# Performance work log

Hardware: AMD Instinct MI355X
Metric: run time of the kernel (lower is better)

Reference implementation:

```python
import jax, jax.numpy as jnp
import numpy as np

S, N, C_M, C_Z, C, H = 256, 384, 64, 128, 32, 8


def _layer_norm(x, w, b, eps=1e-5):
    mu = x.mean(axis=-1, keepdims=True)
    var = x.var(axis=-1, keepdims=True)
    return (x - mu) / jnp.sqrt(var + eps) * w + b


def setup_inputs() -> dict:
    key = jax.random.key(0)
    ks = jax.random.split(key, 8)
    m = jax.random.normal(ks[0], (S, N, C_M), dtype=jnp.float32)
    z = jax.random.normal(ks[1], (N, N, C_Z), dtype=jnp.float32)
    single_mask = jax.random.bernoulli(ks[2], 0.9, (N,))
    scale = 0.02
    return {
        "m": m,
        "z": z,
        "single_mask": single_mask,
        "ln_m_w": jnp.ones((C_M,), jnp.float32),
        "ln_m_b": jnp.zeros((C_M,), jnp.float32),
        "ln_z_w": jnp.ones((C_Z,), jnp.float32),
        "ln_z_b": jnp.zeros((C_Z,), jnp.float32),
        "w_v": jax.random.normal(ks[3], (C_M, H * C), jnp.float32) * scale,
        "w_b": jax.random.normal(ks[4], (C_Z, H), jnp.float32) * scale,
        "w_g": jax.random.normal(ks[5], (C_M, H * C), jnp.float32) * scale,
        "w_out": jax.random.normal(ks[6], (H * C, C_M), jnp.float32) * scale,
    }


def reference(m, z, single_mask, ln_m_w, ln_m_b, ln_z_w, ln_z_b, w_v, w_b, w_g, w_out):
    # m: [s, i, c_m], z: [i, j, c_z], single_mask: [j] bool
    m_ln = _layer_norm(m, ln_m_w, ln_m_b)
    v = (m_ln @ w_v).reshape(S, N, H, C)          # [s, j, h, c]
    b = _layer_norm(z, ln_z_w, ln_z_b) @ w_b      # [i, j, h]
    g = jax.nn.sigmoid(m_ln @ w_g)                # [s, i, h*c]
    # mask broadcast over j axis: [..., None, :, None]
    b = b + jnp.where(single_mask[None, :, None], 0.0, -1e9)
    w = jax.nn.softmax(b, axis=-2)                # softmax over j
    o = jnp.einsum('ijh,sjhc->sihc', w, v)        # [s, i, h, c]
    o = g * o.reshape(S, N, H * C)
    return o @ w_out                               # [s, i, c_m]
```

## Files before the change

kernel.cpp:

```cpp
#include <hip/hip_runtime.h>
#include <math.h>


#define SS 256
#define NN 384
#define CM 64
#define CZ 128
#define HH 8
#define HC 256
#define NV 25165824

typedef __attribute__((ext_vector_type(8))) short short8v;
typedef __attribute__((ext_vector_type(8))) unsigned short ushort8v;
typedef __attribute__((ext_vector_type(4))) unsigned short ushort4v;
typedef __attribute__((ext_vector_type(4))) float f32x4;

static __device__ __forceinline__ float bf2f(unsigned short u) {
    union { unsigned int i; float f; } x; x.i = ((unsigned int)u) << 16; return x.f;
}
static __device__ __forceinline__ unsigned short f2bf(float f) {
    union { float f; unsigned int i; } x; x.f = f;
    unsigned int r = x.i + 0x7FFFu + ((x.i >> 16) & 1u);
    return (unsigned short)(r >> 16);
}
static __device__ __forceinline__ void gload_lds16(const void* g, void* l) {
    __builtin_amdgcn_global_load_lds((const __attribute__((address_space(1))) void*)g,
                                     (__attribute__((address_space(3))) void*)l, 16, 0, 0);
}

__global__ __launch_bounds__(384) void k0_mask(const unsigned int* __restrict__ mu,
                                               float* __restrict__ mterm)
{
    __shared__ int byteLayout;
    if (threadIdx.x == 0) byteLayout = 0;
    __syncthreads();
    if (threadIdx.x < 96) {
        unsigned int u = mu[threadIdx.x];
        if (u != 0u && u != 1u && u != 0x3F800000u) atomicOr(&byteLayout, 1);
    }
    __syncthreads();
    const int j = threadIdx.x;
    int val;
    if (byteLayout) val = ((const unsigned char*)mu)[j];
    else            val = (mu[j] != 0u);
    mterm[j] = val ? 0.0f : -1e9f;
}

__global__ __launch_bounds__(256) void k1a_stageB(
    const float* __restrict__ w_v, const float* __restrict__ w_g,
    unsigned short* __restrict__ BTg)
{
    const int col = blockIdx.x * 4 + (threadIdx.x >> 6);
    const int k   = threadIdx.x & 63;
    float w = (col < 256) ? w_v[k * 256 + col] : w_g[k * 256 + (col - 256)];
    BTg[col * 64 + (k ^ ((col & 7) << 3))] = f2bf(w);
}

__global__ __launch_bounds__(128) void k2a_stageW(
    const float* __restrict__ lnw, const float* __restrict__ lnb, const float* __restrict__ w_b,
    unsigned short* __restrict__ w2bf, float* __restrict__ consts)
{
    __shared__ float pA[128][8], pB[128][8];
    const int c = threadIdx.x;
    float lw = lnw[c], lb = lnb[c];
    float4 wb0 = *(const float4*)&w_b[c * 8];
    float4 wb1 = *(const float4*)&w_b[c * 8 + 4];
    float wv[8] = {wb0.x, wb0.y, wb0.z, wb0.w, wb1.x, wb1.y, wb1.z, wb1.w};
    #pragma unroll
    for (int h = 0; h < 8; h++) {
        w2bf[h * CZ + c]       = f2bf(lw * wv[h]);
        w2bf[(8 + h) * CZ + c] = 0;
        pA[c][h] = lw * wv[h];
        pB[c][h] = lb * wv[h];
    }
    __syncthreads();
    if (c < 8) {
        float A = 0.f, B = 0.f;
        for (int q = 0; q < 128; q++) { A += pA[q][c]; B += pB[q][c]; }
        consts[c] = A; consts[16 + c] = B;
        consts[8 + c] = 0.f; consts[24 + c] = 0.f;
    }
}

__global__ __launch_bounds__(256) void k1n_ln(
    const float* __restrict__ m, const float* __restrict__ lnw, const float* __restrict__ lnb,
    unsigned short* __restrict__ mln)
{
    const int tid = threadIdx.x, wid = tid >> 6, lane = tid & 63;
    const int rowBase = blockIdx.x * 64 + wid * 16;
    const float lw = lnw[lane], lb = lnb[lane];
    #pragma unroll 4
    for (int rr = 0; rr < 16; rr++) {
        int row = rowBase + rr;
        float x = m[(size_t)row * CM + lane];
        float s1 = x, s2 = x * x;
        #pragma unroll
        for (int off = 32; off; off >>= 1) {
            s1 += __shfl_xor(s1, off);
            s2 += __shfl_xor(s2, off);
        }
        float mu  = s1 * (1.0f / CM);
        float var = s2 * (1.0f / CM) - mu * mu;
        float y = (x - mu) * rsqrtf(var + 1e-5f) * lw + lb;
        mln[(size_t)row * CM + (lane ^ ((row & 7) << 3))] = f2bf(y);
    }
}

__global__ __launch_bounds__(256) void k1b_vg(
    const unsigned short* __restrict__ BTg, const unsigned short* __restrict__ mln,
    unsigned short* __restrict__ vT, unsigned short* __restrict__ gout)
{
    __shared__ unsigned short Wl[32768];
    __shared__ unsigned short Al[4096];
    const int tid = threadIdx.x, wid = tid >> 6, lane = tid & 63;
    const int rl = lane & 15, kc = lane >> 4;
    const int rowBase = blockIdx.x * 64;
    const int s = rowBase / NN, j0 = rowBase - s * NN;

    #pragma unroll
    for (int it = 0; it < 16; it++) {
        int eoff = (wid * 16 + it) * 512;
        gload_lds16(BTg + eoff + lane * 8, (void*)((char*)Wl + eoff * 2));
    }
    #pragma unroll
    for (int it = 0; it < 2; it++) {
        int eoff = (wid * 2 + it) * 512;
        gload_lds16(mln + (size_t)rowBase * CM + eoff + lane * 8, (void*)((char*)Al + eoff * 2));
    }
    __syncthreads();

    short8v al[2][4];
    #pragma unroll
    for (int ks = 0; ks < 2; ks++)
        #pragma unroll
        for (int q = 0; q < 4; q++) {
            int row = q * 16 + rl;
            al[ks][q] = *(const short8v*)&Al[(row * 64 + ks * 32 + kc * 8) ^ ((row & 7) << 3)];
        }

    {
        f32x4 acc[4][4] = {};
        #pragma unroll
        for (int ks = 0; ks < 2; ks++) {
            short8v wf[4];
            #pragma unroll
            for (int q = 0; q < 4; q++) {
                int col = wid * 64 + q * 16 + rl;
                wf[q] = *(const short8v*)&Wl[(col * 64 + ks * 32 + kc * 8) ^ ((col & 7) << 3)];
            }
            #pragma unroll
            for (int mi = 0; mi < 4; mi++)
                #pragma unroll
                for (int nf = 0; nf < 4; nf++)
                    acc[mi][nf] = __builtin_amdgcn_mfma_f32_16x16x32_bf16(al[ks][mi], wf[nf], acc[mi][nf], 0, 0, 0);
        }
        #pragma unroll
        for (int mi = 0; mi < 4; mi++) {
            const int jb = j0 + mi * 16 + kc * 4;
            #pragma unroll
            for (int nf = 0; nf < 4; nf++) {
                int hc = wid * 64 + nf * 16 + rl;
                size_t vrow = (size_t)((hc >> 5) * 8192 + s * 32 + (hc & 31));
                ushort4v o4;
                #pragma unroll
                for (int r = 0; r < 4; r++) o4[r] = f2bf(acc[mi][nf][r]);
                *(ushort4v*)&vT[vrow * NN + jb] = o4;
            }
        }
    }

    {
        f32x4 acc[4][4] = {};
        #pragma unroll
        for (int ks = 0; ks < 2; ks++) {
            short8v wf[4];
            #pragma unroll
            for (int q = 0; q < 4; q++) {
                int col = 256 + wid * 64 + q * 16 + rl;
                wf[q] = *(const short8v*)&Wl[(col * 64 + ks * 32 + kc * 8) ^ ((col & 7) << 3)];
            }
            #pragma unroll
            for (int mi = 0; mi < 4; mi++)
                #pragma unroll
                for (int nf = 0; nf < 4; nf++)
                    acc[mi][nf] = __builtin_amdgcn_mfma_f32_16x16x32_bf16(wf[mi], al[ks][nf], acc[mi][nf], 0, 0, 0);
        }
        #pragma unroll
        for (int mi = 0; mi < 4; mi++) {
            const int hcb = wid * 64 + mi * 16 + kc * 4;
            #pragma unroll
            for (int nf = 0; nf < 4; nf++) {
                int row = rowBase + nf * 16 + rl;
                ushort4v o4;
                #pragma unroll
                for (int r = 0; r < 4; r++)
                    o4[r] = f2bf(1.0f / (1.0f + expf(-acc[mi][nf][r])));
                *(ushort4v*)&gout[(size_t)row * HC + hcb] = o4;
            }
        }
    }
}

__global__ __launch_bounds__(256) void k2_mfma(
    const float* __restrict__ z, const unsigned short* __restrict__ w2bf,
    const float* __restrict__ consts, const float* __restrict__ mterm,
    unsigned short* __restrict__ wbl)
{
    __shared__ float st[4][16][2];
    const int tid = threadIdx.x, wid = tid >> 6, lane = tid & 63;
    const int rl = lane & 15, kc = lane >> 4;
    const int rowBase = blockIdx.x * 64 + wid * 16;
    const int i = rowBase / NN, j0 = rowBase - i * NN;
    const float* zr = z + (size_t)(rowBase + rl) * CZ + kc * 8;

    float s1 = 0.f, s2 = 0.f;
    short8v af[4];
    #pragma unroll
    for (int ks = 0; ks < 4; ks++) {
        float4 z0 = *(const float4*)(zr + ks * 32);
        float4 z1 = *(const float4*)(zr + ks * 32 + 4);
        float zz[8] = {z0.x, z0.y, z0.z, z0.w, z1.x, z1.y, z1.z, z1.w};
        short8v a;
        #pragma unroll
        for (int q = 0; q < 8; q++) {
            s1 += zz[q];
            s2 += zz[q] * zz[q];
            a[q] = (short)f2bf(zz[q]);
        }
        af[ks] = a;
    }
    s1 += __shfl_xor(s1, 16); s2 += __shfl_xor(s2, 16);
    s1 += __shfl_xor(s1, 32); s2 += __shfl_xor(s2, 32);
    if (kc == 0) { st[wid][rl][0] = s1; st[wid][rl][1] = s2; }

    f32x4 acc = {};
    #pragma unroll
    for (int ks = 0; ks < 4; ks++) {
        short8v b = *(const short8v*)&w2bf[rl * CZ + ks * 32 + kc * 8];
        acc = __builtin_amdgcn_mfma_f32_16x16x32_bf16(af[ks], b, acc, 0, 0, 0);
    }
    __syncthreads();

    const float Ah = consts[rl], Bh = consts[16 + rl];
    unsigned short pv[4];
    #pragma unroll
    for (int reg = 0; reg < 4; reg++) {
        int r = 4 * kc + reg;
        float S1 = st[wid][r][0], S2 = st[wid][r][1];
        float mu   = S1 * (1.0f / CZ);
        float var  = S2 * (1.0f / CZ) - mu * mu;
        float rstd = rsqrtf(var + 1e-5f);
        float b = rstd * acc[reg] - rstd * mu * Ah + Bh + mterm[j0 + r];
        pv[reg] = f2bf(b);
    }
    if (rl < 8) {
        ushort4v o4 = {pv[0], pv[1], pv[2], pv[3]};
        *(ushort4v*)&wbl[((size_t)rl * NN + i) * NN + j0 + 4 * kc] = o4;
    }
}

__global__ __launch_bounds__(256) void k3_softmax(unsigned short* __restrict__ wbl)
{
    const int tid = threadIdx.x, wave = tid >> 6, lane = tid & 63;
    const int row = blockIdx.x * 4 + wave;
    unsigned short* p = wbl + (size_t)row * NN;
    float x[6];
    float mx = -1e30f;
    #pragma unroll
    for (int e = 0; e < 6; e++) { x[e] = bf2f(p[lane + e * 64]); mx = fmaxf(mx, x[e]); }
    #pragma unroll
    for (int off = 32; off; off >>= 1) mx = fmaxf(mx, __shfl_xor(mx, off));
    float sum = 0.f;
    #pragma unroll
    for (int e = 0; e < 6; e++) { x[e] = expf(x[e] - mx); sum += x[e]; }
    #pragma unroll
    for (int off = 32; off; off >>= 1) sum += __shfl_xor(sum, off);
    float inv = 1.0f / sum;
    #pragma unroll
    for (int e = 0; e < 6; e++) p[lane + e * 64] = f2bf(x[e] * inv);
}

__global__ __launch_bounds__(256) void k4_mfma(
    const unsigned short* __restrict__ wbf, const unsigned short* __restrict__ vT,
    unsigned short* __restrict__ ob)
{
    __shared__ unsigned short Al[128 * 32];
    __shared__ unsigned short Bl[128 * 32];
    const int tid  = threadIdx.x;
    const int wid  = tid >> 6, lane = tid & 63;
    const int wm   = wid >> 1, wn = wid & 1;
    const int h    = blockIdx.z;
    const int i0   = blockIdx.y * 128;
    const int n0   = blockIdx.x * 128;
    const unsigned short* Ag = wbf + (size_t)h * NN * NN;
    const unsigned short* Bg = vT  + (size_t)h * 8192 * NN;

    f32x4 acc[4][4] = {};

    const int lrow = lane >> 2, lchunk = lane & 3;
    for (int k0 = 0; k0 < NN; k0 += 32) {
        #pragma unroll
        for (int q = 0; q < 2; q++) {
            int issue = wid * 2 + q;
            int r = issue * 16 + lrow;
            gload_lds16(Ag + (size_t)(i0 + r) * NN + k0 + lchunk * 8,
                        (void*)((char*)Al + issue * 1024));
            gload_lds16(Bg + (size_t)(n0 + r) * NN + k0 + lchunk * 8,
                        (void*)((char*)Bl + issue * 1024));
        }
        __syncthreads();

        short8v a[4], b[4];
        #pragma unroll
        for (int mi = 0; mi < 4; mi++)
            a[mi] = *(const short8v*)&Al[(wm * 64 + mi * 16 + (lane & 15)) * 32 + (lane >> 4) * 8];
        #pragma unroll
        for (int ni = 0; ni < 4; ni++)
            b[ni] = *(const short8v*)&Bl[(wn * 64 + ni * 16 + (lane & 15)) * 32 + (lane >> 4) * 8];
        #pragma unroll
        for (int mi = 0; mi < 4; mi++)
            #pragma unroll
            for (int ni = 0; ni < 4; ni++)
                acc[mi][ni] = __builtin_amdgcn_mfma_f32_16x16x32_bf16(a[mi], b[ni], acc[mi][ni], 0, 0, 0);
        __syncthreads();
    }

    #pragma unroll
    for (int mi = 0; mi < 4; mi++) {
        const int ibase = i0 + wm * 64 + mi * 16 + ((lane >> 4) << 2);
        #pragma unroll
        for (int ni = 0; ni < 4; ni++) {
            const int n = n0 + wn * 64 + ni * 16 + (lane & 15);
            const int s = n >> 5, c = n & 31;
            #pragma unroll
            for (int r = 0; r < 4; r++)
                ob[((size_t)s * NN + (ibase + r)) * HC + (h << 5) + c] = f2bf(acc[mi][ni][r]);
        }
    }
}

__global__ __launch_bounds__(256) void k5_mfma(
    const unsigned short* __restrict__ ob, const unsigned short* __restrict__ g,
    const float* __restrict__ w_out, float* __restrict__ out)
{
    __shared__ unsigned short WT[64 * 256];
    const int tid = threadIdx.x, wid = tid >> 6, lane = tid & 63;
    #pragma unroll
    for (int e = 0; e < 16; e++) {
        int fidx = (tid + e * 256) * 4;
        float4 w4 = *(const float4*)&w_out[fidx];
        int k = fidx >> 6, c0 = fidx & 63;
        float wv[4] = {w4.x, w4.y, w4.z, w4.w};
        #pragma unroll
        for (int q = 0; q < 4; q++) {
            int c = c0 + q;
            WT[(((c << 8) + k)) ^ ((c & 7) << 3)] = f2bf(wv[q]);
        }
    }
    __syncthreads();

    const size_t rowbase = (size_t)blockIdx.x * 64 + wid * 16;
    const int arow = lane & 15, achunk = lane >> 4;
    const unsigned short* op = ob + (rowbase + arow) * HC + achunk * 8;
    const unsigned short* gp = g  + (rowbase + arow) * HC + achunk * 8;

    f32x4 acc[4] = {};
    #pragma unroll
    for (int ks = 0; ks < 8; ks++) {
        ushort8v o8 = *(const ushort8v*)(op + ks * 32);
        ushort8v g8 = *(const ushort8v*)(gp + ks * 32);
        short8v a;
        #pragma unroll
        for (int q = 0; q < 8; q++)
            a[q] = (short)f2bf(bf2f(o8[q]) * bf2f(g8[q]));
        #pragma unroll
        for (int nf = 0; nf < 4; nf++) {
            const int c = nf * 16 + arow;
            short8v b = *(const short8v*)&WT[(((c << 8) + ks * 32 + achunk * 8)) ^ ((c & 7) << 3)];
            acc[nf] = __builtin_amdgcn_mfma_f32_16x16x32_bf16(a, b, acc[nf], 0, 0, 0);
        }
    }
    #pragma unroll
    for (int nf = 0; nf < 4; nf++)
        #pragma unroll
        for (int r = 0; r < 4; r++)
            out[(rowbase + achunk * 4 + r) * CM + nf * 16 + arow] = acc[nf][r];
}

extern "C" void kernel_launch(void* const* d_in, const int* in_sizes, int n_in,
                              void* d_out, int out_size, void* d_ws, size_t ws_size,
                              hipStream_t stream)
{
    const float* m      = (const float*)d_in[0];
    const float* z      = (const float*)d_in[1];
    const unsigned int* mask_raw = (const unsigned int*)d_in[2];
    const float* ln_m_w = (const float*)d_in[3];
    const float* ln_m_b = (const float*)d_in[4];
    const float* ln_z_w = (const float*)d_in[5];
    const float* ln_z_b = (const float*)d_in[6];
    const float* w_v    = (const float*)d_in[7];
    const float* w_b    = (const float*)d_in[8];
    const float* w_g    = (const float*)d_in[9];
    const float* w_out  = (const float*)d_in[10];
    float* out = (float*)d_out;

    float* mterm = (float*)d_ws;
    unsigned short* wbl = (unsigned short*)(mterm + 384);
    unsigned short* vT  = wbl + 1179648;
    unsigned short* g   = vT + NV;
    unsigned short* ob  = g + NV;
    unsigned short* BTg = ob + NV;
    unsigned short* w2bf = BTg + 32768;
    float* consts = (float*)(w2bf + 2048);
    unsigned short* mln = ob;

    k0_mask<<<1, 384, 0, stream>>>(mask_raw, mterm);
    k1a_stageB<<<128, 256, 0, stream>>>(w_v, w_g, BTg);
    k2a_stageW<<<1, 128, 0, stream>>>(ln_z_w, ln_z_b, w_b, w2bf, consts);
    k1n_ln<<<1536, 256, 0, stream>>>(m, ln_m_w, ln_m_b, mln);
    k1b_vg<<<1536, 256, 0, stream>>>(BTg, mln, vT, g);
    k2_mfma<<<2304, 256, 0, stream>>>(z, w2bf, consts, mterm, wbl);
    k3_softmax<<<768, 256, 0, stream>>>(wbl);
    k4_mfma<<<dim3(64, 3, 8), 256, 0, stream>>>(wbl, vT, ob);
    k5_mfma<<<1536, 256, 0, stream>>>(ob, g, w_out, out);
}
```

Baseline: 140.4 us.

## Stage v/g outputs through LDS for coalesced stores and drop block barrier

Each wave now loads its own slices of the V and G weights plus a redundant full copy of the activation tile. A per-wave vmcnt wait then replaces the block-wide __syncthreads. The V and G GEMM results are transposed through the wave's own already-consumed weight region in LDS, so global writes become 16-byte row-contiguous stores instead of scattered 8-byte ones. The sigmoid also switches to __expf. The cost is extra LDS traffic, redundant loads of the activation tile by every wave, and slightly lower exp precision.

```diff
diff --git a/kernel.cpp b/kernel.cpp
--- a/kernel.cpp
+++ b/kernel.cpp
@@ -118,16 +118,22 @@
     const int s = rowBase / NN, j0 = rowBase - s * NN;
 
     #pragma unroll
-    for (int it = 0; it < 16; it++) {
-        int eoff = (wid * 16 + it) * 512;
+    for (int it = 0; it < 8; it++) {
+        int eoff = wid * 4096 + it * 512;
         gload_lds16(BTg + eoff + lane * 8, (void*)((char*)Wl + eoff * 2));
     }
     #pragma unroll
-    for (int it = 0; it < 2; it++) {
-        int eoff = (wid * 2 + it) * 512;
+    for (int it = 0; it < 8; it++) {
+        int eoff = 16384 + wid * 4096 + it * 512;
+        gload_lds16(BTg + eoff + lane * 8, (void*)((char*)Wl + eoff * 2));
+    }
+    #pragma unroll
+    for (int it = 0; it < 8; it++) {
+        int eoff = it * 512;
         gload_lds16(mln + (size_t)rowBase * CM + eoff + lane * 8, (void*)((char*)Al + eoff * 2));
     }
-    __syncthreads();
+    asm volatile("s_waitcnt vmcnt(0)" ::: "memory");
+    __builtin_amdgcn_sched_barrier(0);
 
     short8v al[2][4];
     #pragma unroll
@@ -137,6 +143,8 @@
             int row = q * 16 + rl;
             al[ks][q] = *(const short8v*)&Al[(row * 64 + ks * 32 + kc * 8) ^ ((row & 7) << 3)];
         }
+
+    unsigned short* VS = Wl + wid * 4096;
 
     {
         f32x4 acc[4][4] = {};
@@ -156,16 +164,24 @@
         }
         #pragma unroll
         for (int mi = 0; mi < 4; mi++) {
-            const int jb = j0 + mi * 16 + kc * 4;
+            const int jb = mi * 16 + kc * 4;
             #pragma unroll
             for (int nf = 0; nf < 4; nf++) {
-                int hc = wid * 64 + nf * 16 + rl;
-                size_t vrow = (size_t)((hc >> 5) * 8192 + s * 32 + (hc & 31));
+                int hcl = nf * 16 + rl;
                 ushort4v o4;
                 #pragma unroll
                 for (int r = 0; r < 4; r++) o4[r] = f2bf(acc[mi][nf][r]);
-                *(ushort4v*)&vT[vrow * NN + jb] = o4;
+                *(ushort4v*)&VS[(hcl * 64 + jb) ^ ((hcl & 7) << 3)] = o4;
             }
+        }
+        #pragma unroll
+        for (int p = 0; p < 8; p++) {
+            int hcl = p * 8 + (lane >> 3);
+            int j8  = (lane & 7) * 8;
+            ushort8v val = *(const ushort8v*)&VS[(hcl * 64 + j8) ^ ((hcl & 7) << 3)];
+            int hc = wid * 64 + hcl;
+            size_t vrow = (size_t)((hc >> 5) * 8192 + s * 32 + (hc & 31));
+            *(ushort8v*)&vT[vrow * NN + j0 + j8] = val;
         }
     }
 
@@ -187,16 +203,23 @@
         }
         #pragma unroll
         for (int mi = 0; mi < 4; mi++) {
-            const int hcb = wid * 64 + mi * 16 + kc * 4;
+            const int hcb = mi * 16 + kc * 4;
             #pragma unroll
             for (int nf = 0; nf < 4; nf++) {
-                int row = rowBase + nf * 16 + rl;
+                int rowl = nf * 16 + rl;
                 ushort4v o4;
                 #pragma unroll
                 for (int r = 0; r < 4; r++)
-                    o4[r] = f2bf(1.0f / (1.0f + expf(-acc[mi][nf][r])));
-                *(ushort4v*)&gout[(size_t)row * HC + hcb] = o4;
+                    o4[r] = f2bf(1.0f / (1.0f + __expf(-acc[mi][nf][r])));
+                *(ushort4v*)&VS[(rowl * 64 + hcb) ^ ((rowl & 7) << 3)] = o4;
             }
+        }
+        #pragma unroll
+        for (int p = 0; p < 8; p++) {
+            int rowl = p * 8 + (lane >> 3);
+            int hc8  = (lane & 7) * 8;
+            ushort8v val = *(const ushort8v*)&VS[(rowl * 64 + hc8) ^ ((rowl & 7) << 3)];
+            *(ushort8v*)&gout[(size_t)(rowBase + rowl) * HC + wid * 64 + hc8] = val;
         }
     }
 }
```

Result: faster. 134.7 us (-4.1%).
